# Optimization experiments

Measured on AMD Instinct MI355X. Metric: run time of the kernel, lower is better.

Reference implementation:

```python
import jax, jax.numpy as jnp
import numpy as np

KERNEL_SIZE = 4
SCALE = 0.5


def setup_inputs() -> dict:
    key = jax.random.key(0)
    k1, k2, k3 = jax.random.split(key, 3)
    M, K, N = 16384, 1024, 4096
    x = jax.random.normal(k1, (M, K), dtype=jnp.float32)
    weight = jax.random.normal(k2, (N, K), dtype=jnp.float32)
    bias = jax.random.normal(k3, (N,), dtype=jnp.float32)
    return {"x": x, "weight": weight, "bias": bias}


def reference(x, weight, bias):
    # y = x @ W^T + b : (M, N)
    y = jnp.einsum('mk,nk->mn', x, weight) + bias[None, :]
    M, N = y.shape
    valid_n = (N // KERNEL_SIZE) * KERNEL_SIZE
    # MaxPool1d(kernel_size, stride=kernel_size): (M, N//k, k) -> max over window
    pooled = jnp.max(y[:, :valid_n].reshape(M, valid_n // KERNEL_SIZE, KERNEL_SIZE), axis=-1)
    # sum over pooled features, then scale -> (M,)
    return jnp.sum(pooled, axis=-1) * SCALE
```

## Files before the change

kernel.cpp:

```cpp
#include <hip/hip_runtime.h>
#include <stdint.h>

#define M_DIM 16384
#define K_DIM 1024
#define N_DIM 4096
#define BM 128
#define BN 128
#define BK 64
#define KT_N (K_DIM / BK)
#define LDSP 40

typedef __bf16 bf16;
typedef __attribute__((ext_vector_type(8))) __bf16 bf16x8;
typedef __attribute__((ext_vector_type(4))) float f32x4;

__device__ __forceinline__ uint32_t pack2_bf16(float a, float b) {
    uint32_t ua = __float_as_uint(a);
    uint32_t ub = __float_as_uint(b);
    ua += 0x7fffu + ((ua >> 16) & 1u);
    ub += 0x7fffu + ((ub >> 16) & 1u);
    return (ua >> 16) | (ub & 0xffff0000u);
}

__device__ __forceinline__ void load_lds16(const bf16* g, bf16* l) {
    __builtin_amdgcn_global_load_lds(
        (__attribute__((address_space(1))) uint32_t*)(uintptr_t)g,
        (__attribute__((address_space(3))) uint32_t*)(uintptr_t)l,
        16, 0, 0);
}

__global__ __launch_bounds__(256) void convert_swizzle_kernel(
    const float* __restrict__ x, const float* __restrict__ w,
    uint4* __restrict__ xsw, uint4* __restrict__ wsw, int xchunks, int wchunks)
{
    int i = blockIdx.x * 256 + threadIdx.x;
    const float* src;
    uint4* dst;
    int idx;
    if (i < xchunks) { src = x; dst = xsw; idx = i; }
    else             { src = w; dst = wsw; idx = i - xchunks; if (idx >= wchunks) return; }

    int e = idx << 3;
    int m = e >> 10;
    int k = e & (K_DIM - 1);
    int mt = m >> 7, r = m & 127;
    int kt = k >> 6;
    int c  = (k >> 3) & 7;
    int tile = mt * KT_N + kt;
    int dstoff = tile * 8192 + r * 64 + ((c ^ (r & 7)) << 3);

    const float4* p = (const float4*)(src + e);
    float4 a = p[0], b = p[1];
    uint4 out;
    out.x = pack2_bf16(a.x, a.y);
    out.y = pack2_bf16(a.z, a.w);
    out.z = pack2_bf16(b.x, b.y);
    out.w = pack2_bf16(b.z, b.w);
    dst[dstoff >> 3] = out;
}

__global__ __launch_bounds__(256) void gemm_pool_sw_kernel(
    const bf16* __restrict__ xb, const bf16* __restrict__ wb,
    const float* __restrict__ bias, float* __restrict__ out)
{
    __shared__ bf16 sA[BM * BK];
    __shared__ bf16 sB[BN * BK];

    const int tid = threadIdx.x;
    const int bx = blockIdx.x;
    const int by = blockIdx.y;

    const int lane = tid & 63;
    const int wave = tid >> 6;
    const int wm = wave >> 1;
    const int wn = wave & 1;
    const int lr = lane & 15;
    const int quad = lane >> 4;

    const bf16* Atile0 = xb + (size_t)(by * KT_N) * 8192 + wave * 2048 + lane * 8;
    const bf16* Btile0 = wb + (size_t)(bx * KT_N) * 8192 + wave * 2048 + lane * 8;
    bf16* ldsA = sA + wave * 2048;
    bf16* ldsB = sB + wave * 2048;

    f32x4 acc[4][4] = {};

    for (int kt = 0; kt < KT_N; ++kt) {
        const bf16* ga = Atile0 + kt * 8192;
        const bf16* gb = Btile0 + kt * 8192;
        #pragma unroll
        for (int q = 0; q < 4; ++q) {
            load_lds16(ga + q * 512, ldsA + q * 512);
            load_lds16(gb + q * 512, ldsB + q * 512);
        }
        __syncthreads();

        #pragma unroll
        for (int s = 0; s < 2; ++s) {
            bf16x8 af[4], bfr[4];
            #pragma unroll
            for (int i = 0; i < 4; ++i) {
                int row = wm * 64 + i * 16 + lr;
                int pos = (s * 4 + quad) ^ (row & 7);
                af[i] = *(const bf16x8*)(sA + row * 64 + pos * 8);
            }
            #pragma unroll
            for (int j = 0; j < 4; ++j) {
                int row = wn * 64 + j * 16 + lr;
                int pos = (s * 4 + quad) ^ (row & 7);
                bfr[j] = *(const bf16x8*)(sB + row * 64 + pos * 8);
            }
            #pragma unroll
            for (int i = 0; i < 4; ++i)
                #pragma unroll
                for (int j = 0; j < 4; ++j)
                    acc[i][j] = __builtin_amdgcn_mfma_f32_16x16x32_bf16(af[i], bfr[j], acc[i][j], 0, 0, 0);
        }
        __syncthreads();
    }

    float bv[4];
    #pragma unroll
    for (int j = 0; j < 4; ++j)
        bv[j] = bias[bx * BN + wn * 64 + j * 16 + lr];

    #pragma unroll
    for (int i = 0; i < 4; ++i) {
        float rs[4] = {0.f, 0.f, 0.f, 0.f};
        #pragma unroll
        for (int j = 0; j < 4; ++j) {
            #pragma unroll
            for (int r = 0; r < 4; ++r) {
                float t = acc[i][j][r] + bv[j];
                t = fmaxf(t, __shfl_xor(t, 1, 64));
                t = fmaxf(t, __shfl_xor(t, 2, 64));
                rs[r] += t;
            }
        }
        #pragma unroll
        for (int r = 0; r < 4; ++r) {
            rs[r] += __shfl_xor(rs[r], 4, 64);
            rs[r] += __shfl_xor(rs[r], 8, 64);
        }
        if (lr == 0) {
            const int row = by * BM + wm * 64 + i * 16 + quad * 4;
            #pragma unroll
            for (int r = 0; r < 4; ++r)
                atomicAdd(&out[row + r], rs[r] * 0.5f);
        }
    }
}

__global__ __launch_bounds__(256) void fused_linear_pool_kernel(
    const float* __restrict__ x, const float* __restrict__ wt,
    const float* __restrict__ bias, float* __restrict__ out)
{
    __shared__ uint32_t sA[BM * LDSP / 2];
    __shared__ uint32_t sB[BN * LDSP / 2];

    const int tid = threadIdx.x;
    const int bx = blockIdx.x;
    const int by = blockIdx.y;

    const float* Abase = x  + (size_t)by * BM * K_DIM;
    const float* Bbase = wt + (size_t)bx * BN * K_DIM;

    const int lane = tid & 63;
    const int wave = tid >> 6;
    const int wm = wave >> 1;
    const int wn = wave & 1;
    const int lr = lane & 15;
    const int quad = lane >> 4;

    const int srow  = tid >> 2;
    const int scol  = (tid & 3) * 8;
    const int swidx = (tid & 3) * 4;

    f32x4 acc[4][4] = {};

    for (int kt = 0; kt < K_DIM; kt += 32) {
        #pragma unroll
        for (int p = 0; p < 2; ++p) {
            const int r = srow + p * 64;
            const float4* ga = (const float4*)(Abase + (size_t)r * K_DIM + kt + scol);
            const float4* gb = (const float4*)(Bbase + (size_t)r * K_DIM + kt + scol);
            float4 a0 = ga[0], a1 = ga[1], b0 = gb[0], b1 = gb[1];
            uint4 wa;
            wa.x = pack2_bf16(a0.x, a0.y); wa.y = pack2_bf16(a0.z, a0.w);
            wa.z = pack2_bf16(a1.x, a1.y); wa.w = pack2_bf16(a1.z, a1.w);
            *(uint4*)&sA[r * (LDSP / 2) + swidx] = wa;
            uint4 wbv;
            wbv.x = pack2_bf16(b0.x, b0.y); wbv.y = pack2_bf16(b0.z, b0.w);
            wbv.z = pack2_bf16(b1.x, b1.y); wbv.w = pack2_bf16(b1.z, b1.w);
            *(uint4*)&sB[r * (LDSP / 2) + swidx] = wbv;
        }
        __syncthreads();

        bf16x8 af[4], bfr[4];
        #pragma unroll
        for (int i = 0; i < 4; ++i)
            af[i] = *(const bf16x8*)((const bf16*)sA + (wm * 64 + i * 16 + lr) * LDSP + quad * 8);
        #pragma unroll
        for (int j = 0; j < 4; ++j)
            bfr[j] = *(const bf16x8*)((const bf16*)sB + (wn * 64 + j * 16 + lr) * LDSP + quad * 8);

        #pragma unroll
        for (int i = 0; i < 4; ++i)
            #pragma unroll
            for (int j = 0; j < 4; ++j)
                acc[i][j] = __builtin_amdgcn_mfma_f32_16x16x32_bf16(af[i], bfr[j], acc[i][j], 0, 0, 0);
        __syncthreads();
    }

    float bv[4];
    #pragma unroll
    for (int j = 0; j < 4; ++j)
        bv[j] = bias[bx * BN + wn * 64 + j * 16 + lr];

    #pragma unroll
    for (int i = 0; i < 4; ++i) {
        float rsum[4] = {0.f, 0.f, 0.f, 0.f};
        #pragma unroll
        for (int j = 0; j < 4; ++j) {
            #pragma unroll
            for (int r = 0; r < 4; ++r) {
                float t = acc[i][j][r] + bv[j];
                t = fmaxf(t, __shfl_xor(t, 1, 64));
                t = fmaxf(t, __shfl_xor(t, 2, 64));
                t += __shfl_xor(t, 4, 64);
                t += __shfl_xor(t, 8, 64);
                rsum[r] += t;
            }
        }
        if (lr == 0) {
            const int row = by * BM + wm * 64 + i * 16 + quad * 4;
            #pragma unroll
            for (int r = 0; r < 4; ++r)
                atomicAdd(&out[row + r], rsum[r] * 0.5f);
        }
    }
}

extern "C" void kernel_launch(void* const* d_in, const int* in_sizes, int n_in,
                              void* d_out, int out_size, void* d_ws, size_t ws_size,
                              hipStream_t stream) {
    const float* x  = (const float*)d_in[0];
    const float* wt = (const float*)d_in[1];
    const float* bs = (const float*)d_in[2];
    float* out = (float*)d_out;

    hipMemsetAsync(out, 0, (size_t)out_size * sizeof(float), stream);

    const size_t xe = (size_t)M_DIM * K_DIM;
    const size_t we = (size_t)N_DIM * K_DIM;
    const size_t need = (xe + we) * sizeof(bf16);

    dim3 grid(N_DIM / BN, M_DIM / BM);

    if (ws_size >= need) {
        bf16* xb = (bf16*)d_ws;
        bf16* wb = xb + xe;
        const int xchunks = (int)(xe / 8);
        const int wchunks = (int)(we / 8);
        const int total   = xchunks + wchunks;
        convert_swizzle_kernel<<<(total + 255) / 256, 256, 0, stream>>>(
            x, wt, (uint4*)xb, (uint4*)wb, xchunks, wchunks);
        gemm_pool_sw_kernel<<<grid, 256, 0, stream>>>(xb, wb, bs, out);
    } else {
        fused_linear_pool_kernel<<<grid, 256, 0, stream>>>(x, wt, bs, out);
    }
}
```

Before: 296.2 us.

## Pre-pack operands in MFMA fragment order and load directly to registers

The conversion kernel now writes x and W in bf16 using a layout that matches the MFMA fragments: each 16-row by 32-k slab is stored so every lane's 8-element fragment is one contiguous 16-byte chunk. The GEMM kernel drops LDS staging and barriers and reads fragments straight from global memory into registers. This removes the LDS traffic and the syncthreads, and the loop is unrolled by 2. In exchange there is no cross-wave data sharing through LDS, so each wave issues its own global loads, with more reliance on L2 and more exposed load latency since there is no explicit prefetch.

```diff
diff --git a/kernel.cpp b/kernel.cpp
--- a/kernel.cpp
+++ b/kernel.cpp
@@ -6,9 +6,12 @@
 #define N_DIM 4096
 #define BM 128
 #define BN 128
-#define BK 64
-#define KT_N (K_DIM / BK)
 #define LDSP 40
+
+#define TILE_ELEMS (128 * K_DIM)
+#define SLAB_ELEMS (128 * 32)
+#define NSLAB_X ((M_DIM / 128) * 32)
+#define NSLAB_W ((N_DIM / 128) * 32)
 
 typedef __bf16 bf16;
 typedef __attribute__((ext_vector_type(8))) __bf16 bf16x8;
@@ -22,100 +25,86 @@
     return (ua >> 16) | (ub & 0xffff0000u);
 }
 
-__device__ __forceinline__ void load_lds16(const bf16* g, bf16* l) {
-    __builtin_amdgcn_global_load_lds(
-        (__attribute__((address_space(1))) uint32_t*)(uintptr_t)g,
-        (__attribute__((address_space(3))) uint32_t*)(uintptr_t)l,
-        16, 0, 0);
-}
-
-__global__ __launch_bounds__(256) void convert_swizzle_kernel(
+__global__ __launch_bounds__(256) void convert_pack_kernel(
     const float* __restrict__ x, const float* __restrict__ w,
-    uint4* __restrict__ xsw, uint4* __restrict__ wsw, int xchunks, int wchunks)
+    bf16* __restrict__ xp, bf16* __restrict__ wp)
 {
-    int i = blockIdx.x * 256 + threadIdx.x;
+    int slab = blockIdx.x;
     const float* src;
-    uint4* dst;
-    int idx;
-    if (i < xchunks) { src = x; dst = xsw; idx = i; }
-    else             { src = w; dst = wsw; idx = i - xchunks; if (idx >= wchunks) return; }
-
-    int e = idx << 3;
-    int m = e >> 10;
-    int k = e & (K_DIM - 1);
-    int mt = m >> 7, r = m & 127;
-    int kt = k >> 6;
-    int c  = (k >> 3) & 7;
-    int tile = mt * KT_N + kt;
-    int dstoff = tile * 8192 + r * 64 + ((c ^ (r & 7)) << 3);
-
-    const float4* p = (const float4*)(src + e);
-    float4 a = p[0], b = p[1];
-    uint4 out;
-    out.x = pack2_bf16(a.x, a.y);
-    out.y = pack2_bf16(a.z, a.w);
-    out.z = pack2_bf16(b.x, b.y);
-    out.w = pack2_bf16(b.z, b.w);
-    dst[dstoff >> 3] = out;
-}
-
-__global__ __launch_bounds__(256) void gemm_pool_sw_kernel(
-    const bf16* __restrict__ xb, const bf16* __restrict__ wb,
+    bf16* dst;
+    if (slab < NSLAB_X) { src = x; dst = xp; }
+    else                { slab -= NSLAB_X; src = w; dst = wp; }
+    const int tile = slab >> 5;
+    const int s    = slab & 31;
+
+    __shared__ uint32_t ls[128 * 16];
+
+    const int t = threadIdx.x;
+    {
+        const int r  = t >> 1;
+        const int kh = (t & 1) * 16;
+        const float4* p = (const float4*)(src + (size_t)(tile * 128 + r) * K_DIM + s * 32 + kh);
+        float4 a = p[0], b = p[1], c = p[2], d = p[3];
+        uint32_t* lrow = &ls[r * 16 + (kh >> 1)];
+        lrow[0] = pack2_bf16(a.x, a.y);
+        lrow[1] = pack2_bf16(a.z, a.w);
+        lrow[2] = pack2_bf16(b.x, b.y);
+        lrow[3] = pack2_bf16(b.z, b.w);
+        lrow[4] = pack2_bf16(c.x, c.y);
+        lrow[5] = pack2_bf16(c.z, c.w);
+        lrow[6] = pack2_bf16(d.x, d.y);
+        lrow[7] = pack2_bf16(d.z, d.w);
+    }
+    __syncthreads();
+    uint4* dst4 = (uint4*)(dst + (size_t)tile * TILE_ELEMS + (size_t)s * SLAB_ELEMS);
+    #pragma unroll
+    for (int p = 0; p < 2; ++p) {
+        const int c   = t + p * 256;
+        const int lane = c & 63;
+        const int rb   = c >> 6;
+        const int q    = lane >> 4;
+        const int lrow = lane & 15;
+        const int r    = rb * 16 + lrow;
+        const uint32_t* lp = &ls[r * 16 + q * 4];
+        uint4 v;
+        v.x = lp[0]; v.y = lp[1]; v.z = lp[2]; v.w = lp[3];
+        dst4[c] = v;
+    }
+}
+
+__global__ __launch_bounds__(256) void gemm_pool_direct_kernel(
+    const bf16* __restrict__ xp, const bf16* __restrict__ wp,
     const float* __restrict__ bias, float* __restrict__ out)
 {
-    __shared__ bf16 sA[BM * BK];
-    __shared__ bf16 sB[BN * BK];
-
-    const int tid = threadIdx.x;
     const int bx = blockIdx.x;
     const int by = blockIdx.y;
 
-    const int lane = tid & 63;
-    const int wave = tid >> 6;
+    const int lane = threadIdx.x & 63;
+    const int wave = threadIdx.x >> 6;
     const int wm = wave >> 1;
     const int wn = wave & 1;
     const int lr = lane & 15;
     const int quad = lane >> 4;
 
-    const bf16* Atile0 = xb + (size_t)(by * KT_N) * 8192 + wave * 2048 + lane * 8;
-    const bf16* Btile0 = wb + (size_t)(bx * KT_N) * 8192 + wave * 2048 + lane * 8;
-    bf16* ldsA = sA + wave * 2048;
-    bf16* ldsB = sB + wave * 2048;
+    const bf16* Abase = xp + (size_t)by * TILE_ELEMS + (wm * 4) * 512 + lane * 8;
+    const bf16* Bbase = wp + (size_t)bx * TILE_ELEMS + (wn * 4) * 512 + lane * 8;
 
     f32x4 acc[4][4] = {};
 
-    for (int kt = 0; kt < KT_N; ++kt) {
-        const bf16* ga = Atile0 + kt * 8192;
-        const bf16* gb = Btile0 + kt * 8192;
-        #pragma unroll
-        for (int q = 0; q < 4; ++q) {
-            load_lds16(ga + q * 512, ldsA + q * 512);
-            load_lds16(gb + q * 512, ldsB + q * 512);
-        }
-        __syncthreads();
-
-        #pragma unroll
-        for (int s = 0; s < 2; ++s) {
-            bf16x8 af[4], bfr[4];
-            #pragma unroll
-            for (int i = 0; i < 4; ++i) {
-                int row = wm * 64 + i * 16 + lr;
-                int pos = (s * 4 + quad) ^ (row & 7);
-                af[i] = *(const bf16x8*)(sA + row * 64 + pos * 8);
-            }
-            #pragma unroll
-            for (int j = 0; j < 4; ++j) {
-                int row = wn * 64 + j * 16 + lr;
-                int pos = (s * 4 + quad) ^ (row & 7);
-                bfr[j] = *(const bf16x8*)(sB + row * 64 + pos * 8);
-            }
-            #pragma unroll
-            for (int i = 0; i < 4; ++i)
-                #pragma unroll
-                for (int j = 0; j < 4; ++j)
-                    acc[i][j] = __builtin_amdgcn_mfma_f32_16x16x32_bf16(af[i], bfr[j], acc[i][j], 0, 0, 0);
-        }
-        __syncthreads();
+    #pragma unroll 2
+    for (int s = 0; s < 32; ++s) {
+        const bf16* ga = Abase + s * SLAB_ELEMS;
+        const bf16* gb = Bbase + s * SLAB_ELEMS;
+        bf16x8 af[4], bfr[4];
+        #pragma unroll
+        for (int i = 0; i < 4; ++i) af[i]  = *(const bf16x8*)(ga + i * 512);
+        #pragma unroll
+        for (int j = 0; j < 4; ++j) bfr[j] = *(const bf16x8*)(gb + j * 512);
+        #pragma unroll
+        for (int i = 0; i < 4; ++i)
+            #pragma unroll
+            for (int j = 0; j < 4; ++j)
+                acc[i][j] = __builtin_amdgcn_mfma_f32_16x16x32_bf16(af[i], bfr[j], acc[i][j], 0, 0, 0);
     }
 
     float bv[4];
@@ -257,14 +246,10 @@
     dim3 grid(N_DIM / BN, M_DIM / BM);
 
     if (ws_size >= need) {
-        bf16* xb = (bf16*)d_ws;
-        bf16* wb = xb + xe;
-        const int xchunks = (int)(xe / 8);
-        const int wchunks = (int)(we / 8);
-        const int total   = xchunks + wchunks;
-        convert_swizzle_kernel<<<(total + 255) / 256, 256, 0, stream>>>(
-            x, wt, (uint4*)xb, (uint4*)wb, xchunks, wchunks);
-        gemm_pool_sw_kernel<<<grid, 256, 0, stream>>>(xb, wb, bs, out);
+        bf16* xp = (bf16*)d_ws;
+        bf16* wp = xp + xe;
+        convert_pack_kernel<<<NSLAB_X + NSLAB_W, 256, 0, stream>>>(x, wt, xp, wp);
+        gemm_pool_direct_kernel<<<grid, 256, 0, stream>>>(xp, wp, bs, out);
     } else {
         fused_linear_pool_kernel<<<grid, 256, 0, stream>>>(x, wt, bs, out);
     }
```

Measured after the change: 295.5 us. No clear change (-0.3%).
